# Kernel optimization log

Hardware: AMD Instinct MI355X
Metric: run time of the kernel (lower is better)

Reference implementation:

```python
import jax, jax.numpy as jnp
import numpy as np

N = 65536
E = 1048576
IN_DIM = 128
POS_DIM = 128  # num_nodes (ROI one-hot dim)
HID = 128


def _mk_params(key):
    # layer 0: local in = IN_DIM + POS_DIM; layer 1: local in = HID + POS_DIM
    dims = [(IN_DIM + POS_DIM, HID), (HID + POS_DIM, HID)]
    params = {}
    for l, (din, _) in enumerate(dims):
        ks = jax.random.split(jax.random.fold_in(key, l), 4)
        params[f"l{l}_lw1"] = jax.random.normal(ks[0], (din, HID), jnp.float32) * (1.0 / np.sqrt(din))
        params[f"l{l}_lb1"] = jnp.zeros((HID,), jnp.float32)
        params[f"l{l}_lw2"] = jax.random.normal(ks[1], (HID, HID), jnp.float32) * (1.0 / np.sqrt(HID))
        params[f"l{l}_lb2"] = jnp.zeros((HID,), jnp.float32)
        params[f"l{l}_gw1"] = jax.random.normal(ks[2], (HID, HID), jnp.float32) * (1.0 / np.sqrt(HID))
        params[f"l{l}_gb1"] = jnp.zeros((HID,), jnp.float32)
        params[f"l{l}_gw2"] = jax.random.normal(ks[3], (HID, HID), jnp.float32) * (1.0 / np.sqrt(HID))
        params[f"l{l}_gb2"] = jnp.zeros((HID,), jnp.float32)
    return params


def setup_inputs() -> dict:
    key = jax.random.key(0)
    k1, k2, k3, k4 = jax.random.split(key, 4)
    inp = {
        "x": jax.random.normal(k1, (N, IN_DIM), jnp.float32),
        "pos": jax.random.normal(k2, (N, POS_DIM), jnp.float32),
        "edge_index": jax.random.randint(k3, (2, E), 0, N, jnp.int64),
    }
    inp.update(_mk_params(k4))
    return inp


def _pointnet_conv(x, pos, src, dst, lw1, lb1, lw2, lb2, gw1, gb1, gw2, gb2):
    # message: concat(x_j, pos_j - pos_i) per edge -> local_nn (Lin-ReLU-Lin)
    msg = jnp.concatenate([x[src], pos[src] - pos[dst]], axis=1)  # [E', in+pos]
    h = jax.nn.relu(msg @ lw1 + lb1) @ lw2 + lb2                  # [E', HID]
    agg = jax.ops.segment_max(h, dst, num_segments=N)             # max aggr (PointNetConv default)
    return jax.nn.relu(agg @ gw1 + gb1) @ gw2 + gb2               # global_nn


def reference(x, pos, edge_index,
              l0_lw1, l0_lb1, l0_lw2, l0_lb2, l0_gw1, l0_gb1, l0_gw2, l0_gb2,
              l1_lw1, l1_lb1, l1_lw2, l1_lb2, l1_gw1, l1_gb1, l1_gw2, l1_gb2):
    # add_self_loops=True (PointNetConv default); ensures every node has an incoming edge
    loops = jnp.arange(N, dtype=edge_index.dtype)
    src = jnp.concatenate([edge_index[0], loops])
    dst = jnp.concatenate([edge_index[1], loops])
    h = _pointnet_conv(x, pos, src, dst, l0_lw1, l0_lb1, l0_lw2, l0_lb2,
                       l0_gw1, l0_gb1, l0_gw2, l0_gb2)
    h = _pointnet_conv(h, pos, src, dst, l1_lw1, l1_lb1, l1_lw2, l1_lb2,
                       l1_gw1, l1_gb1, l1_gw2, l1_gb2)
    return h
```

## Files before the change

kernel.cpp:

```cpp
#include <hip/hip_runtime.h>
#include <hip/hip_bf16.h>
#include <stdint.h>

#define NN 65536
#define NE 1048576
#define E2 (NE + NN)
#define HID 128
#define LP 136
#define RMAX 13
#define TP 129
#define TABW 1680
#define ENC_NEG 0x007FFFFFu

typedef _Float16 h8v __attribute__((ext_vector_type(8)));
typedef __fp16 fp16x2 __attribute__((ext_vector_type(2)));
typedef __attribute__((ext_vector_type(4))) float f32x4;

__device__ __forceinline__ uint32_t pkh(float a, float b){
    union { fp16x2 h; uint32_t u; } v;
    v.h = __builtin_amdgcn_cvt_pkrtz(a, b);
    return v.u;
}
__device__ __forceinline__ uint32_t encf(float x){
    union { float f; uint32_t u; } v; v.f = x;
    return v.u ^ (uint32_t)(((int32_t)v.u >> 31) | 0x80000000);
}
__device__ __forceinline__ float decf(uint32_t u){
    union { uint32_t u; float f; } v;
    v.u = u ^ (uint32_t)(~((int32_t)u >> 31) | 0x80000000);
    return v.f;
}

__device__ __forceinline__ void gl_lds16(const _Float16* g, _Float16* l){
    __builtin_amdgcn_global_load_lds(
        (const __attribute__((address_space(1))) uint32_t*)g,
        (__attribute__((address_space(3))) uint32_t*)l, 16, 0, 0);
}

__device__ __forceinline__ void dma_w(const _Float16* __restrict__ wT, _Float16* Ws,
                                      int wv, int lane){
    #pragma unroll
    for (int rnd = 0; rnd < 8; rnd++){
        int g = rnd*256 + wv*64 + lane;
        int r = g >> 4, kc = g & 15;
        gl_lds16(wT + r*HID + ((kc ^ (r & 15)) << 3),
                 Ws + rnd*2048 + wv*512);
    }
}

__device__ __forceinline__ void gemm64(const _Float16* Ts, const _Float16* Ws,
                                       f32x4 (&acc)[8], int wv, int lq, int quad){
    #pragma unroll
    for (int k0 = 0; k0 < 128; k0 += 32){
        h8v af = *(const h8v*)(Ts + (wv*16 + lq)*LP + k0 + quad*8);
        const int kcb = k0 >> 3;
        #pragma unroll
        for (int ct = 0; ct < 8; ct++){
            h8v b = *(const h8v*)(Ws + (ct*16 + lq)*128 + (((kcb + quad) ^ lq) << 3));
            acc[ct] = __builtin_amdgcn_mfma_f32_16x16x32_f16(af, b, acc[ct], 0, 0, 0);
        }
    }
}

__device__ __forceinline__ void zero_acc8(f32x4 (&acc)[8]){
    #pragma unroll
    for (int b = 0; b < 8; b++) acc[b] = (f32x4){0.f, 0.f, 0.f, 0.f};
}

__device__ __forceinline__ void zero_acc(f32x4 (&acc)[2][8]){
    #pragma unroll
    for (int a = 0; a < 2; a++)
        #pragma unroll
        for (int b = 0; b < 8; b++)
            acc[a][b] = (f32x4){0.f, 0.f, 0.f, 0.f};
}

struct WT { const float* s[10]; _Float16* d[10]; };
__global__ void k_prep(WT w, uint32_t* cnt,
                       const float* lb2_0, const float* gw1_0, const float* gb1_0,
                       const float* lb2_1, const float* gw1_1, const float* gb1_1,
                       float* c1p){
    int b = blockIdx.x;
    if (b < 640){
        int m = b >> 6;
        int t = (b & 63) * 256 + threadIdx.x;
        int n = t >> 7, k = t & 127;
        w.d[m][n*128 + k] = (_Float16)w.s[m][k*128 + n];
    } else if (b < 896){
        cnt[(b - 640)*256 + threadIdx.x] = 1u;
    } else {
        int l = b - 896;
        int j = threadIdx.x;
        if (j < 128){
            const float* lb2 = l ? lb2_1 : lb2_0;
            const float* gw1 = l ? gw1_1 : gw1_0;
            float s = (l ? gb1_1 : gb1_0)[j];
            for (int k = 0; k < 128; k++) s += lb2[k] * gw1[k*128 + j];
            c1p[l*128 + j] = s;
        }
    }
}

__launch_bounds__(256, 3)
__global__ void k_histab3(const int* __restrict__ ei, uint32_t* __restrict__ cnt,
                          const float* __restrict__ x, const float* __restrict__ pos,
                          const _Float16* __restrict__ w1aT0, const _Float16* __restrict__ w1bT0,
                          const _Float16* __restrict__ w1bT1, const float* __restrict__ lb1_0,
                          _Float16* __restrict__ Ah, _Float16* __restrict__ Bh0,
                          _Float16* __restrict__ Bh1, uint32_t* __restrict__ agg){
    __shared__ _Float16 Ts[64*LP];
    __shared__ _Float16 Ws[128*128];
    __shared__ float b1s[128];
    const int tid = threadIdx.x;

    if (blockIdx.x >= 1024){
        int e = (blockIdx.x - 1024) * 256 + tid;
        atomicAdd(&cnt[ei[NE + e]], 1u);
        return;
    }

    const int node0 = blockIdx.x * 64;
    const int wv = tid >> 6, lane = tid & 63, lq = lane & 15, quad = lane >> 4;
    if (tid < 128) b1s[tid] = lb1_0[tid];

    {
        uint4* ap = (uint4*)(agg + (size_t)node0 * HID);
        uint4 v = make_uint4(ENC_NEG, ENC_NEG, ENC_NEG, ENC_NEG);
        #pragma unroll
        for (int i = 0; i < 8; i++) ap[tid + i*256] = v;
    }
    #pragma unroll
    for (int i = 0; i < 8; i++){
        int chunk = tid + i*256;
        int row = chunk >> 5, qc = chunk & 31;
        float4 f = *(const float4*)(pos + (size_t)(node0 + row)*HID + qc*4);
        uint2 o; o.x = pkh(f.x, f.y); o.y = pkh(f.z, f.w);
        *(uint2*)(Ts + row*LP + qc*4) = o;
    }
    dma_w(w1bT0, Ws, wv, lane);
    __syncthreads();

    f32x4 acc0[8], acc1[8];
    zero_acc8(acc0);
    gemm64(Ts, Ws, acc0, wv, lq, quad);
    __syncthreads();
    dma_w(w1bT1, Ws, wv, lane);
    #pragma unroll
    for (int ct = 0; ct < 8; ct++)
        #pragma unroll
        for (int rg = 0; rg < 4; rg++)
            Bh0[(size_t)(node0 + wv*16 + quad*4 + rg)*HID + ct*16 + lq]
                = (_Float16)acc0[ct][rg];
    __syncthreads();

    zero_acc8(acc1);
    gemm64(Ts, Ws, acc1, wv, lq, quad);
    __syncthreads();

    #pragma unroll
    for (int i = 0; i < 8; i++){
        int chunk = tid + i*256;
        int row = chunk >> 5, qc = chunk & 31;
        float4 f = *(const float4*)(x + (size_t)(node0 + row)*HID + qc*4);
        uint2 o; o.x = pkh(f.x, f.y); o.y = pkh(f.z, f.w);
        *(uint2*)(Ts + row*LP + qc*4) = o;
    }
    dma_w(w1aT0, Ws, wv, lane);
    #pragma unroll
    for (int ct = 0; ct < 8; ct++)
        #pragma unroll
        for (int rg = 0; rg < 4; rg++)
            Bh1[(size_t)(node0 + wv*16 + quad*4 + rg)*HID + ct*16 + lq]
                = (_Float16)acc1[ct][rg];
    __syncthreads();

    gemm64(Ts, Ws, acc0, wv, lq, quad);

    #pragma unroll
    for (int ct = 0; ct < 8; ct++)
        #pragma unroll
        for (int rg = 0; rg < 4; rg++){
            int c = ct*16 + lq;
            Ah[(size_t)(node0 + wv*16 + quad*4 + rg)*HID + c]
                = (_Float16)(acc0[ct][rg] + b1s[c]);
        }
}

__global__ void k_scan1(const uint32_t* __restrict__ cnt, uint32_t* __restrict__ bsum){
    __shared__ uint32_t ps[256];
    int t = threadIdx.x;
    ps[t] = cnt[blockIdx.x*256 + t]; __syncthreads();
    for (int off = 128; off > 0; off >>= 1){
        if (t < off) ps[t] += ps[t + off];
        __syncthreads();
    }
    if (t == 0) bsum[blockIdx.x] = ps[0];
}
__global__ void k_scan23(const uint32_t* __restrict__ cnt, const uint32_t* __restrict__ bsum,
                         uint32_t* __restrict__ cur){
    __shared__ uint32_t ps[256];
    __shared__ uint32_t bs[256];
    int t = threadIdx.x, b = blockIdx.x, i = b*256 + t;
    uint32_t bb = bsum[b];
    bs[t] = bsum[t];
    uint32_t v = cnt[i];
    ps[t] = v; __syncthreads();
    for (int off = 1; off < 256; off <<= 1){
        uint32_t u = (t >= off) ? ps[t - off] : 0u;
        uint32_t w = (t >= off) ? bs[t - off] : 0u;
        __syncthreads();
        ps[t] += u; bs[t] += w;
        __syncthreads();
    }
    cur[i] = (bs[b] - bb) + ps[t] - v;
}
__global__ void k_scatter(const int* __restrict__ ei, uint32_t* cur,
                          uint2* __restrict__ sedge){
    int e = blockIdx.x * 256 + threadIdx.x;
    if (e >= E2) return;
    uint32_t s, d;
    if (e < NE){ s = (uint32_t)ei[e]; d = (uint32_t)ei[NE + e]; }
    else { s = d = (uint32_t)(e - NE); }
    uint32_t p = atomicAdd(&cur[d], 1u);
    sedge[p] = make_uint2(s, d);
}

__launch_bounds__(256, 4)
__global__ void k_edge(const uint2* __restrict__ sedge,
                       const _Float16* __restrict__ Ah, const _Float16* __restrict__ Bh,
                       const _Float16* __restrict__ w2T,
                       uint32_t* __restrict__ agg){
    __shared__ _Float16 Ws[128*128];
    __shared__ __align__(16) uint32_t tab[TABW];
    __shared__ int ds_s[128];
    __shared__ unsigned long long masks_s[2];
    __shared__ int run_dst_s[RMAX];
    const int tid = threadIdx.x;
    const int bid = blockIdx.x;
    const int lb  = (bid & 7) * (E2/128/8) + (bid >> 3);
    const int e0 = lb * 128;
    const int wv = tid >> 6, lane = tid & 63, lq = lane & 15, quad = lane >> 4;
    const int r0 = wv*32 + lq, r1 = r0 + 16;

    const uint2 ea = sedge[e0 + r0];
    const uint2 eb = sedge[e0 + r1];
    int d_cur = 0;
    if (tid < 128) d_cur = (int)sedge[e0 + tid].y;

    dma_w(w2T, Ws, wv, lane);

    const _Float16* a0p = Ah + (size_t)ea.x*HID + quad*8;
    const _Float16* a1p = Ah + (size_t)eb.x*HID + quad*8;
    const _Float16* b0p = Bh + (size_t)ea.y*HID + quad*8;
    const _Float16* b1p = Bh + (size_t)eb.y*HID + quad*8;
    h8v A0[4], A1[4], B0[4], B1[4];
    #pragma unroll
    for (int i = 0; i < 4; i++){
        A0[i] = *(const h8v*)(a0p + 32*i);
        A1[i] = *(const h8v*)(a1p + 32*i);
        B0[i] = *(const h8v*)(b0p + 32*i);
        B1[i] = *(const h8v*)(b1p + 32*i);
    }

    bool flag = false;
    if (tid < 128){
        ds_s[tid] = d_cur;
        int d_up  = __shfl_up(d_cur, 1);
        int d_b63 = __shfl((int)eb.y, 15);
        if (tid & 63) flag = (d_cur != d_up);
        else          flag = (tid == 0) ? true : (d_cur != d_b63);
        unsigned long long m = __ballot(flag);
        if ((tid & 63) == 0) masks_s[tid >> 6] = m;
    }
    {
        uint4* t4 = (uint4*)tab;
        const uint4 vneg = make_uint4(ENC_NEG, ENC_NEG, ENC_NEG, ENC_NEG);
        #pragma unroll
        for (int i = 0; i < 2; i++){
            int idx = tid + i*256;
            if (idx < TABW/4) t4[idx] = vneg;
        }
    }
    __syncthreads();

    const unsigned long long m0 = masks_s[0], m1 = masks_s[1];
    const int c0 = __popcll(m0);
    const int nruns = c0 + __popcll(m1);

    if (flag){
        int r;
        if (tid < 64) r = __popcll(m0 & ((2ull << tid) - 1)) - 1;
        else          r = c0 + __popcll(m1 & ((2ull << (tid-64)) - 1)) - 1;
        if (r < RMAX) run_dst_s[r] = d_cur;
    }

    f32x4 acc[2][8];
    zero_acc(acc);

    const h8v zero8 = (h8v)(_Float16)0;
    #pragma unroll
    for (int i = 0; i < 4; i++){
        h8v a0 = __builtin_elementwise_max(A0[i] - B0[i], zero8);
        h8v a1 = __builtin_elementwise_max(A1[i] - B1[i], zero8);
        const int kcb = i*4;
        #pragma unroll
        for (int ct = 0; ct < 8; ct++){
            h8v b = *(const h8v*)(Ws + (ct*16 + lq)*128 + (((kcb + quad) ^ lq) << 3));
            acc[0][ct] = __builtin_amdgcn_mfma_f32_16x16x32_f16(a0, b, acc[0][ct], 0, 0, 0);
            acc[1][ct] = __builtin_amdgcn_mfma_f32_16x16x32_f16(a1, b, acc[1][ct], 0, 0, 0);
        }
    }

    #pragma unroll
    for (int rt = 0; rt < 2; rt++){
        const int rb = wv*32 + rt*16 + quad*4;
        int rid[4];
        #pragma unroll
        for (int i = 0; i < 4; i++){
            int r = rb + i;
            if (r < 64) rid[i] = __popcll(m0 & ((2ull << r) - 1)) - 1;
            else        rid[i] = c0 + __popcll(m1 & ((2ull << (r-64)) - 1)) - 1;
        }
        const bool b01 = rid[1] != rid[0];
        const bool b12 = rid[2] != rid[1];
        const bool b23 = rid[3] != rid[2];
        #pragma unroll
        for (int ct = 0; ct < 8; ct++){
            const int c = ct*16 + lq;
            float v0 = acc[rt][ct][0], v1 = acc[rt][ct][1];
            float v2 = acc[rt][ct][2], v3 = acc[rt][ct][3];
            #define FLUSH(ID, R, V) do{ uint32_t ev = encf(V); \
                if (__builtin_expect((ID) < RMAX, 1)) atomicMax(&tab[(ID)*TP + c], ev); \
                else atomicMax(&agg[(size_t)ds_s[R]*HID + c], ev); }while(0)
            if (b01) FLUSH(rid[0], rb+0, v0); else v1 = fmaxf(v1, v0);
            if (b12) FLUSH(rid[1], rb+1, v1); else v2 = fmaxf(v2, v1);
            if (b23) FLUSH(rid[2], rb+2, v2); else v3 = fmaxf(v3, v2);
            FLUSH(rid[3], rb+3, v3);
            #undef FLUSH
        }
    }
    __syncthreads();

    {
        const int c = tid & 127;
        const int ntab = nruns < RMAX ? nruns : RMAX;
        for (int r = tid >> 7; r < ntab; r += 2){
            uint32_t v = tab[r*TP + c];
            uint32_t* dst = &agg[(size_t)run_dst_s[r]*HID + c];
            if (r == 0 || r == nruns-1 || nruns > RMAX) atomicMax(dst, v);
            else *dst = v;
        }
    }
}

__launch_bounds__(256, 3)
__global__ void k_gnn_ab(uint32_t* __restrict__ agg,
                         const _Float16* __restrict__ g1T, const _Float16* __restrict__ g2T,
                         const float* __restrict__ c1p, const float* __restrict__ gb2,
                         const _Float16* __restrict__ w1aT1, const _Float16* __restrict__ Bh1,
                         const float* __restrict__ lb1_1,
                         _Float16* __restrict__ Ah){
    __shared__ _Float16 Ts[64*LP];
    __shared__ _Float16 Ws[128*128];
    __shared__ float c1s[128];
    __shared__ float c2s[128];
    __shared__ float b1s[128];
    const int tid = threadIdx.x;
    const int node0 = blockIdx.x * 64;
    const int wv = tid >> 6, lane = tid & 63, lq = lane & 15, quad = lane >> 4;
    if (tid < 128){ c1s[tid] = c1p[tid]; c2s[tid] = gb2[tid]; b1s[tid] = lb1_1[tid]; }

    {
        const uint4 vneg = make_uint4(ENC_NEG, ENC_NEG, ENC_NEG, ENC_NEG);
        #pragma unroll
        for (int i = 0; i < 8; i++){
            int chunk = tid + i*256;
            int row = chunk >> 5, qc = chunk & 31;
            uint4* ga = (uint4*)(agg + (size_t)(node0 + row)*HID + qc*4);
            uint4 u = *ga; *ga = vneg;
            uint2 o; o.x = pkh(decf(u.x), decf(u.y)); o.y = pkh(decf(u.z), decf(u.w));
            *(uint2*)(Ts + row*LP + qc*4) = o;
        }
    }
    dma_w(g1T, Ws, wv, lane);
    __syncthreads();

    f32x4 acc[8];
    zero_acc8(acc);
    gemm64(Ts, Ws, acc, wv, lq, quad);
    __syncthreads();
    dma_w(g2T, Ws, wv, lane);
    #pragma unroll
    for (int ct = 0; ct < 8; ct++)
        #pragma unroll
        for (int rg = 0; rg < 4; rg++){
            int c = ct*16 + lq;
            Ts[(wv*16 + quad*4 + rg)*LP + c] = (_Float16)fmaxf(acc[ct][rg] + c1s[c], 0.f);
        }
    __syncthreads();

    zero_acc8(acc);
    gemm64(Ts, Ws, acc, wv, lq, quad);
    __syncthreads();
    dma_w(w1aT1, Ws, wv, lane);
    #pragma unroll
    for (int ct = 0; ct < 8; ct++)
        #pragma unroll
        for (int rg = 0; rg < 4; rg++){
            int c = ct*16 + lq;
            Ts[(wv*16 + quad*4 + rg)*LP + c] = (_Float16)(acc[ct][rg] + c2s[c]);
        }
    __syncthreads();

    _Float16 bres[8][4];
    #pragma unroll
    for (int ct = 0; ct < 8; ct++)
        #pragma unroll
        for (int rg = 0; rg < 4; rg++)
            bres[ct][rg] = Bh1[(size_t)(node0 + wv*16 + quad*4 + rg)*HID + ct*16 + lq];

    zero_acc8(acc);
    gemm64(Ts, Ws, acc, wv, lq, quad);

    #pragma unroll
    for (int ct = 0; ct < 8; ct++)
        #pragma unroll
        for (int rg = 0; rg < 4; rg++){
            int c = ct*16 + lq;
            float v = acc[ct][rg] + (float)bres[ct][rg] + b1s[c];
            Ah[(size_t)(node0 + wv*16 + quad*4 + rg)*HID + c] = (_Float16)v;
        }
}

__launch_bounds__(256, 3)
__global__ void k_gnn(const uint32_t* __restrict__ agg,
                      const _Float16* __restrict__ g1T, const _Float16* __restrict__ g2T,
                      const float* __restrict__ c1p, const float* __restrict__ gb2,
                      float* __restrict__ outf){
    __shared__ _Float16 Ts[64*LP];
    __shared__ _Float16 Ws[128*128];
    __shared__ float c1s[128];
    __shared__ float c2s[128];
    const int tid = threadIdx.x;
    const int node0 = blockIdx.x * 64;
    const int wv = tid >> 6, lane = tid & 63, lq = lane & 15, quad = lane >> 4;
    if (tid < 128){ c1s[tid] = c1p[tid]; c2s[tid] = gb2[tid]; }

    {
        #pragma unroll
        for (int i = 0; i < 8; i++){
            int chunk = tid + i*256;
            int row = chunk >> 5, qc = chunk & 31;
            const uint4* ga = (const uint4*)(agg + (size_t)(node0 + row)*HID + qc*4);
            uint4 u = *ga;
            uint2 o; o.x = pkh(decf(u.x), decf(u.y)); o.y = pkh(decf(u.z), decf(u.w));
            *(uint2*)(Ts + row*LP + qc*4) = o;
        }
    }
    dma_w(g1T, Ws, wv, lane);
    __syncthreads();

    f32x4 acc[8];
    zero_acc8(acc);
    gemm64(Ts, Ws, acc, wv, lq, quad);
    __syncthreads();
    dma_w(g2T, Ws, wv, lane);
    #pragma unroll
    for (int ct = 0; ct < 8; ct++)
        #pragma unroll
        for (int rg = 0; rg < 4; rg++){
            int c = ct*16 + lq;
            Ts[(wv*16 + quad*4 + rg)*LP + c] = (_Float16)fmaxf(acc[ct][rg] + c1s[c], 0.f);
        }
    __syncthreads();

    zero_acc8(acc);
    gemm64(Ts, Ws, acc, wv, lq, quad);

    #pragma unroll
    for (int ct = 0; ct < 8; ct++)
        #pragma unroll
        for (int rg = 0; rg < 4; rg++){
            int c = ct*16 + lq;
            outf[(size_t)(node0 + wv*16 + quad*4 + rg)*HID + c] = acc[ct][rg] + c2s[c];
        }
}

extern "C" void kernel_launch(void* const* d_in, const int* in_sizes, int n_in,
                              void* d_out, int out_size, void* d_ws, size_t ws_size,
                              hipStream_t stream){
    const float* x   = (const float*)d_in[0];
    const float* pos = (const float*)d_in[1];
    const int*   ei  = (const int*)d_in[2];
    const float* W[16];
    for (int i = 0; i < 16; i++) W[i] = (const float*)d_in[3 + i];

    uint8_t* p = (uint8_t*)d_ws;
    _Float16* wT[10];
    for (int i = 0; i < 10; i++) wT[i] = (_Float16*)(p + (size_t)i * 32768);
    size_t off = 10 * 32768;
    _Float16* Ah  = (_Float16*)(p + off); off += (size_t)NN * HID * 2;
    _Float16* Bh0 = (_Float16*)(p + off); off += (size_t)NN * HID * 2;
    _Float16* Bh1 = (_Float16*)(p + off); off += (size_t)NN * HID * 2;
    uint32_t* agg = (uint32_t*)(p + off); off += (size_t)NN * HID * 4;
    uint32_t* cnt = (uint32_t*)(p + off); off += (size_t)NN * 4;
    uint32_t* cur = (uint32_t*)(p + off); off += (size_t)NN * 4;
    uint32_t* bsum = (uint32_t*)(p + off); off += 256 * 4;
    uint32_t* bofs = (uint32_t*)(p + off); off += 256 * 4;
    float* c1p = (float*)(p + off); off += 256 * 4;
    uint2* sedge = (uint2*)(p + off); off += (size_t)E2 * 8;
    (void)ws_size; (void)in_sizes; (void)n_in; (void)out_size; (void)bofs;

    WT wt;
    for (int l = 0; l < 2; l++){
        wt.s[5*l + 0] = W[8*l + 0];
        wt.s[5*l + 1] = W[8*l + 0] + 128*128;
        wt.s[5*l + 2] = W[8*l + 2];
        wt.s[5*l + 3] = W[8*l + 4];
        wt.s[5*l + 4] = W[8*l + 6];
        for (int j = 0; j < 5; j++) wt.d[5*l + j] = wT[5*l + j];
    }
    k_prep<<<898, 256, 0, stream>>>(wt, cnt, W[3], W[4], W[5], W[11], W[12], W[13], c1p);

    k_histab3<<<1024 + NE/256, 256, 0, stream>>>(ei, cnt, x, pos, wT[0], wT[1], wT[6],
                                                 W[1], Ah, Bh0, Bh1, agg);
    k_scan1<<<256, 256, 0, stream>>>(cnt, bsum);
    k_scan23<<<256, 256, 0, stream>>>(cnt, bsum, cur);
    k_scatter<<<(E2 + 255)/256, 256, 0, stream>>>(ei, cur, sedge);

    k_edge<<<E2/128, 256, 0, stream>>>(sedge, Ah, Bh0, wT[2], agg);
    k_gnn_ab<<<NN/64, 256, 0, stream>>>(agg, wT[3], wT[4], c1p, W[7],
                                        wT[5], Bh1, W[9], Ah);
    k_edge<<<E2/128, 256, 0, stream>>>(sedge, Ah, Bh1, wT[7], agg);
    k_gnn<<<NN/64, 256, 0, stream>>>(agg, wT[8], wT[9], c1p + 128, W[15],
                                     (float*)d_out);
}
```

Baseline: 452.4 us.

## Double node tile per block to 128 rows with 512-thread blocks sharing weights

The per-node GEMM kernels (histogram/A-B precompute, the gnn_ab kernel and the final gnn kernel) now process 128 nodes per block with 8 waves instead of 64 nodes with 4 waves. Each 128x128 weight tile loaded into LDS is reused across twice as many rows, halving the weight DMA traffic per node. In k_histab3 the two pos GEMMs are reordered so one accumulator array is reused, which lowers register pressure. The cost is larger LDS use per block and a launch bound of (512, 4) that may cap registers, with the risk of spills or lower occupancy.

```diff
diff --git a/kernel.cpp b/kernel.cpp
--- a/kernel.cpp
+++ b/kernel.cpp
@@ -47,8 +47,18 @@
                  Ws + rnd*2048 + wv*512);
     }
 }
-
-__device__ __forceinline__ void gemm64(const _Float16* Ts, const _Float16* Ws,
+__device__ __forceinline__ void dma_w8(const _Float16* __restrict__ wT, _Float16* Ws,
+                                       int wv, int lane){
+    #pragma unroll
+    for (int rnd = 0; rnd < 4; rnd++){
+        int g = rnd*512 + wv*64 + lane;
+        int r = g >> 4, kc = g & 15;
+        gl_lds16(wT + r*HID + ((kc ^ (r & 15)) << 3),
+                 Ws + rnd*4096 + wv*512);
+    }
+}
+
+__device__ __forceinline__ void gemm_w(const _Float16* Ts, const _Float16* Ws,
                                        f32x4 (&acc)[8], int wv, int lq, int quad){
     #pragma unroll
     for (int k0 = 0; k0 < 128; k0 += 32){
@@ -101,25 +111,25 @@
     }
 }
 
-__launch_bounds__(256, 3)
+__launch_bounds__(512, 4)
 __global__ void k_histab3(const int* __restrict__ ei, uint32_t* __restrict__ cnt,
                           const float* __restrict__ x, const float* __restrict__ pos,
                           const _Float16* __restrict__ w1aT0, const _Float16* __restrict__ w1bT0,
                           const _Float16* __restrict__ w1bT1, const float* __restrict__ lb1_0,
                           _Float16* __restrict__ Ah, _Float16* __restrict__ Bh0,
                           _Float16* __restrict__ Bh1, uint32_t* __restrict__ agg){
-    __shared__ _Float16 Ts[64*LP];
+    __shared__ _Float16 Ts[128*LP];
     __shared__ _Float16 Ws[128*128];
     __shared__ float b1s[128];
     const int tid = threadIdx.x;
 
-    if (blockIdx.x >= 1024){
-        int e = (blockIdx.x - 1024) * 256 + tid;
+    if (blockIdx.x >= 512){
+        int e = (blockIdx.x - 512) * 512 + tid;
         atomicAdd(&cnt[ei[NE + e]], 1u);
         return;
     }
 
-    const int node0 = blockIdx.x * 64;
+    const int node0 = blockIdx.x * 128;
     const int wv = tid >> 6, lane = tid & 63, lq = lane & 15, quad = lane >> 4;
     if (tid < 128) b1s[tid] = lb1_0[tid];
 
@@ -127,54 +137,58 @@
         uint4* ap = (uint4*)(agg + (size_t)node0 * HID);
         uint4 v = make_uint4(ENC_NEG, ENC_NEG, ENC_NEG, ENC_NEG);
         #pragma unroll
-        for (int i = 0; i < 8; i++) ap[tid + i*256] = v;
-    }
-    #pragma unroll
-    for (int i = 0; i < 8; i++){
-        int chunk = tid + i*256;
-        int row = chunk >> 5, qc = chunk & 31;
-        float4 f = *(const float4*)(pos + (size_t)(node0 + row)*HID + qc*4);
-        uint2 o; o.x = pkh(f.x, f.y); o.y = pkh(f.z, f.w);
-        *(uint2*)(Ts + row*LP + qc*4) = o;
-    }
-    dma_w(w1bT0, Ws, wv, lane);
-    __syncthreads();
-
-    f32x4 acc0[8], acc1[8];
-    zero_acc8(acc0);
-    gemm64(Ts, Ws, acc0, wv, lq, quad);
-    __syncthreads();
-    dma_w(w1bT1, Ws, wv, lane);
+        for (int i = 0; i < 8; i++) ap[tid + i*512] = v;
+    }
+    #pragma unroll
+    for (int i = 0; i < 4; i++){
+        int chunk = tid + i*512;
+        int row = chunk >> 4, qc = chunk & 15;
+        const float4* src = (const float4*)(pos + (size_t)(node0 + row)*HID + qc*8);
+        float4 f0 = src[0], f1 = src[1];
+        uint4 o; o.x = pkh(f0.x, f0.y); o.y = pkh(f0.z, f0.w);
+        o.z = pkh(f1.x, f1.y); o.w = pkh(f1.z, f1.w);
+        *(uint4*)(Ts + row*LP + qc*8) = o;
+    }
+    dma_w8(w1bT1, Ws, wv, lane);
+    __syncthreads();
+
+    f32x4 acc[8];
+    zero_acc8(acc);
+    gemm_w(Ts, Ws, acc, wv, lq, quad);
+    __syncthreads();
+    dma_w8(w1bT0, Ws, wv, lane);
+    #pragma unroll
+    for (int ct = 0; ct < 8; ct++)
+        #pragma unroll
+        for (int rg = 0; rg < 4; rg++)
+            Bh1[(size_t)(node0 + wv*16 + quad*4 + rg)*HID + ct*16 + lq]
+                = (_Float16)acc[ct][rg];
+    __syncthreads();
+
+    zero_acc8(acc);
+    gemm_w(Ts, Ws, acc, wv, lq, quad);
+    __syncthreads();
+
+    #pragma unroll
+    for (int i = 0; i < 4; i++){
+        int chunk = tid + i*512;
+        int row = chunk >> 4, qc = chunk & 15;
+        const float4* src = (const float4*)(x + (size_t)(node0 + row)*HID + qc*8);
+        float4 f0 = src[0], f1 = src[1];
+        uint4 o; o.x = pkh(f0.x, f0.y); o.y = pkh(f0.z, f0.w);
+        o.z = pkh(f1.x, f1.y); o.w = pkh(f1.z, f1.w);
+        *(uint4*)(Ts + row*LP + qc*8) = o;
+    }
+    dma_w8(w1aT0, Ws, wv, lane);
     #pragma unroll
     for (int ct = 0; ct < 8; ct++)
         #pragma unroll
         for (int rg = 0; rg < 4; rg++)
             Bh0[(size_t)(node0 + wv*16 + quad*4 + rg)*HID + ct*16 + lq]
-                = (_Float16)acc0[ct][rg];
-    __syncthreads();
-
-    zero_acc8(acc1);
-    gemm64(Ts, Ws, acc1, wv, lq, quad);
-    __syncthreads();
-
-    #pragma unroll
-    for (int i = 0; i < 8; i++){
-        int chunk = tid + i*256;
-        int row = chunk >> 5, qc = chunk & 31;
-        float4 f = *(const float4*)(x + (size_t)(node0 + row)*HID + qc*4);
-        uint2 o; o.x = pkh(f.x, f.y); o.y = pkh(f.z, f.w);
-        *(uint2*)(Ts + row*LP + qc*4) = o;
-    }
-    dma_w(w1aT0, Ws, wv, lane);
-    #pragma unroll
-    for (int ct = 0; ct < 8; ct++)
-        #pragma unroll
-        for (int rg = 0; rg < 4; rg++)
-            Bh1[(size_t)(node0 + wv*16 + quad*4 + rg)*HID + ct*16 + lq]
-                = (_Float16)acc1[ct][rg];
-    __syncthreads();
-
-    gemm64(Ts, Ws, acc0, wv, lq, quad);
+                = (_Float16)acc[ct][rg];
+    __syncthreads();
+
+    gemm_w(Ts, Ws, acc, wv, lq, quad);
 
     #pragma unroll
     for (int ct = 0; ct < 8; ct++)
@@ -182,7 +196,7 @@
         for (int rg = 0; rg < 4; rg++){
             int c = ct*16 + lq;
             Ah[(size_t)(node0 + wv*16 + quad*4 + rg)*HID + c]
-                = (_Float16)(acc0[ct][rg] + b1s[c]);
+                = (_Float16)(acc[ct][rg] + b1s[c]);
         }
 }
 
@@ -353,20 +367,20 @@
     }
 }
 
-__launch_bounds__(256, 3)
+__launch_bounds__(512, 4)
 __global__ void k_gnn_ab(uint32_t* __restrict__ agg,
                          const _Float16* __restrict__ g1T, const _Float16* __restrict__ g2T,
                          const float* __restrict__ c1p, const float* __restrict__ gb2,
                          const _Float16* __restrict__ w1aT1, const _Float16* __restrict__ Bh1,
                          const float* __restrict__ lb1_1,
                          _Float16* __restrict__ Ah){
-    __shared__ _Float16 Ts[64*LP];
+    __shared__ _Float16 Ts[128*LP];
     __shared__ _Float16 Ws[128*128];
     __shared__ float c1s[128];
     __shared__ float c2s[128];
     __shared__ float b1s[128];
     const int tid = threadIdx.x;
-    const int node0 = blockIdx.x * 64;
+    const int node0 = blockIdx.x * 128;
     const int wv = tid >> 6, lane = tid & 63, lq = lane & 15, quad = lane >> 4;
     if (tid < 128){ c1s[tid] = c1p[tid]; c2s[tid] = gb2[tid]; b1s[tid] = lb1_1[tid]; }
 
@@ -374,7 +388,7 @@
         const uint4 vneg = make_uint4(ENC_NEG, ENC_NEG, ENC_NEG, ENC_NEG);
         #pragma unroll
         for (int i = 0; i < 8; i++){
-            int chunk = tid + i*256;
+            int chunk = tid + i*512;
             int row = chunk >> 5, qc = chunk & 31;
             uint4* ga = (uint4*)(agg + (size_t)(node0 + row)*HID + qc*4);
             uint4 u = *ga; *ga = vneg;
@@ -382,14 +396,14 @@
             *(uint2*)(Ts + row*LP + qc*4) = o;
         }
     }
-    dma_w(g1T, Ws, wv, lane);
+    dma_w8(g1T, Ws, wv, lane);
     __syncthreads();
 
     f32x4 acc[8];
     zero_acc8(acc);
-    gemm64(Ts, Ws, acc, wv, lq, quad);
-    __syncthreads();
-    dma_w(g2T, Ws, wv, lane);
+    gemm_w(Ts, Ws, acc, wv, lq, quad);
+    __syncthreads();
+    dma_w8(g2T, Ws, wv, lane);
     #pragma unroll
     for (int ct = 0; ct < 8; ct++)
         #pragma unroll
@@ -400,9 +414,9 @@
     __syncthreads();
 
     zero_acc8(acc);
-    gemm64(Ts, Ws, acc, wv, lq, quad);
-    __syncthreads();
-    dma_w(w1aT1, Ws, wv, lane);
+    gemm_w(Ts, Ws, acc, wv, lq, quad);
+    __syncthreads();
+    dma_w8(w1aT1, Ws, wv, lane);
     #pragma unroll
     for (int ct = 0; ct < 8; ct++)
         #pragma unroll
@@ -420,7 +434,7 @@
             bres[ct][rg] = Bh1[(size_t)(node0 + wv*16 + quad*4 + rg)*HID + ct*16 + lq];
 
     zero_acc8(acc);
-    gemm64(Ts, Ws, acc, wv, lq, quad);
+    gemm_w(Ts, Ws, acc, wv, lq, quad);
 
     #pragma unroll
     for (int ct = 0; ct < 8; ct++)
@@ -432,24 +446,24 @@
         }
 }
 
-__launch_bounds__(256, 3)
+__launch_bounds__(512, 4)
 __global__ void k_gnn(const uint32_t* __restrict__ agg,
                       const _Float16* __restrict__ g1T, const _Float16* __restrict__ g2T,
                       const float* __restrict__ c1p, const float* __restrict__ gb2,
                       float* __restrict__ outf){
-    __shared__ _Float16 Ts[64*LP];
+    __shared__ _Float16 Ts[128*LP];
     __shared__ _Float16 Ws[128*128];
     __shared__ float c1s[128];
     __shared__ float c2s[128];
     const int tid = threadIdx.x;
-    const int node0 = blockIdx.x * 64;
+    const int node0 = blockIdx.x * 128;
     const int wv = tid >> 6, lane = tid & 63, lq = lane & 15, quad = lane >> 4;
     if (tid < 128){ c1s[tid] = c1p[tid]; c2s[tid] = gb2[tid]; }
 
     {
         #pragma unroll
         for (int i = 0; i < 8; i++){
-            int chunk = tid + i*256;
+            int chunk = tid + i*512;
             int row = chunk >> 5, qc = chunk & 31;
             const uint4* ga = (const uint4*)(agg + (size_t)(node0 + row)*HID + qc*4);
             uint4 u = *ga;
@@ -457,14 +471,14 @@
             *(uint2*)(Ts + row*LP + qc*4) = o;
         }
     }
-    dma_w(g1T, Ws, wv, lane);
+    dma_w8(g1T, Ws, wv, lane);
     __syncthreads();
 
     f32x4 acc[8];
     zero_acc8(acc);
-    gemm64(Ts, Ws, acc, wv, lq, quad);
-    __syncthreads();
-    dma_w(g2T, Ws, wv, lane);
+    gemm_w(Ts, Ws, acc, wv, lq, quad);
+    __syncthreads();
+    dma_w8(g2T, Ws, wv, lane);
     #pragma unroll
     for (int ct = 0; ct < 8; ct++)
         #pragma unroll
@@ -475,7 +489,7 @@
     __syncthreads();
 
     zero_acc8(acc);
-    gemm64(Ts, Ws, acc, wv, lq, quad);
+    gemm_w(Ts, Ws, acc, wv, lq, quad);
 
     #pragma unroll
     for (int ct = 0; ct < 8; ct++)
@@ -522,16 +536,16 @@
     }
     k_prep<<<898, 256, 0, stream>>>(wt, cnt, W[3], W[4], W[5], W[11], W[12], W[13], c1p);
 
-    k_histab3<<<1024 + NE/256, 256, 0, stream>>>(ei, cnt, x, pos, wT[0], wT[1], wT[6],
-                                                 W[1], Ah, Bh0, Bh1, agg);
+    k_histab3<<<512 + NE/512, 512, 0, stream>>>(ei, cnt, x, pos, wT[0], wT[1], wT[6],
+                                                W[1], Ah, Bh0, Bh1, agg);
     k_scan1<<<256, 256, 0, stream>>>(cnt, bsum);
     k_scan23<<<256, 256, 0, stream>>>(cnt, bsum, cur);
     k_scatter<<<(E2 + 255)/256, 256, 0, stream>>>(ei, cur, sedge);
 
     k_edge<<<E2/128, 256, 0, stream>>>(sedge, Ah, Bh0, wT[2], agg);
-    k_gnn_ab<<<NN/64, 256, 0, stream>>>(agg, wT[3], wT[4], c1p, W[7],
-                                        wT[5], Bh1, W[9], Ah);
+    k_gnn_ab<<<NN/128, 512, 0, stream>>>(agg, wT[3], wT[4], c1p, W[7],
+                                         wT[5], Bh1, W[9], Ah);
     k_edge<<<E2/128, 256, 0, stream>>>(sedge, Ah, Bh1, wT[7], agg);
-    k_gnn<<<NN/64, 256, 0, stream>>>(agg, wT[8], wT[9], c1p + 128, W[15],
-                                     (float*)d_out);
-}
+    k_gnn<<<NN/128, 512, 0, stream>>>(agg, wT[8], wT[9], c1p + 128, W[15],
+                                      (float*)d_out);
+}
```

Result: no change. 450.0 us (-0.5%).
